# Performance work log

Hardware: AMD Instinct MI355X
Metric: run time of the kernel (lower is better)

Reference implementation:

```python
import jax, jax.numpy as jnp
import numpy as np

NEG_INF = -1e30

def setup_inputs() -> dict:
    key = jax.random.key(0)
    k1, k2, k3, k4, k5 = jax.random.split(key, 5)
    B, S, D, A = 16, 1024, 1024, 256
    hidden = jax.random.normal(k1, (B, S, D), dtype=jnp.float32)
    W1 = jax.random.normal(k2, (D, A), dtype=jnp.float32) / np.sqrt(D)
    b1 = jax.random.normal(k3, (A,), dtype=jnp.float32) * 0.01
    v = jax.random.normal(k4, (A,), dtype=jnp.float32) / np.sqrt(A)
    prompt_type_ids = jax.random.randint(k5, (B,), 0, 3, dtype=jnp.int32)
    return {"hidden": hidden, "W1": W1, "b1": b1, "v": v,
            "prompt_type_ids": prompt_type_ids}

def reference(hidden, W1, b1, v, prompt_type_ids):
    # hidden: [B,S,D]; per-token variable-length context attention pooling.
    B, S, D = hidden.shape
    # scores depend only on the context token l, not on the query position j
    attn_in = jnp.tanh(jnp.einsum('bsd,da->bsa', hidden, W1) + b1)  # [B,S,A]
    scores = jnp.einsum('bsa,a->bs', attn_in, v)                    # [B,S]

    idx = jnp.arange(S)
    j = idx[:, None]   # query position
    l = idx[None, :]   # context position
    prefix_m = l <= j          # h[:j+1]
    postfix_m = l >= j         # h[j:]
    cloze_m = l != j           # leave-one-out
    pt = prompt_type_ids[:, None, None]                              # [B,1,1]
    mask = jnp.where(pt == 0, prefix_m[None],
                     jnp.where(pt == 1, postfix_m[None], cloze_m[None]))  # [B,S,S] bool

    masked_scores = jnp.where(mask, scores[:, None, :], NEG_INF)    # [B,S(j),S(l)]
    p = jax.nn.softmax(masked_scores, axis=-1)                      # softmax over context
    cnt = jnp.sum(mask, axis=-1).astype(hidden.dtype)               # context length L per (b,j)
    # output = (1/L) * sum_l p_l * h_l  (the original's mean of p_l*h_l rows)
    pooled = jnp.einsum('bjl,bld->bjd', p, hidden) / cnt[..., None]
    return pooled
```

## Files before the change

### kernel.cpp

```cpp
#include <hip/hip_runtime.h>
#include <math.h>

#define SS 1024
#define DD 1024
#define AA 256
#define BB 16

typedef short short8 __attribute__((ext_vector_type(8)));
typedef short short4v __attribute__((ext_vector_type(4)));
typedef float f32x4 __attribute__((ext_vector_type(4)));

static __device__ __forceinline__ short f2bf(float f) {
    union { float f; unsigned u; } x; x.f = f;
    unsigned r = x.u + 0x7FFFu + ((x.u >> 16) & 1u);
    return (short)(r >> 16);
}

__global__ __launch_bounds__(256) void w1cvt_kernel(
    const float* __restrict__ W1, short* __restrict__ W1f)
{
    const int g  = blockIdx.x * 256 + threadIdx.x;
    const int l  = g & 63;
    const int nb = (g >> 6) & 15;
    const int kb = g >> 10;
    const int k0 = kb * 32 + ((l >> 4) << 3);
    const int n  = nb * 16 + (l & 15);
    short8 o;
    #pragma unroll
    for (int j = 0; j < 8; ++j) o[j] = f2bf(W1[(size_t)(k0 + j) * AA + n]);
    *reinterpret_cast<short8*>(&W1f[(size_t)g * 8]) = o;
}

__global__ __launch_bounds__(256) void scores_mfma_kernel(
    const float* __restrict__ hidden, const short* __restrict__ W1f,
    const float* __restrict__ b1, const float* __restrict__ v,
    float* __restrict__ scores)
{
    __shared__ short A_lds[32 * 32];
    __shared__ float red[4][32];

    const int tid = threadIdx.x;
    const int w   = tid >> 6;
    const int l   = tid & 63;
    const int row0 = blockIdx.x * 32;

    const int sr = tid >> 3;
    const int sc = (tid & 7) * 4;
    const float* hsrc = hidden + (size_t)(row0 + sr) * DD + sc;

    f32x4 acc[2][4];
    #pragma unroll
    for (int m = 0; m < 2; ++m)
        #pragma unroll
        for (int nb = 0; nb < 4; ++nb)
            #pragma unroll
            for (int r = 0; r < 4; ++r) acc[m][nb][r] = 0.f;

    const int a_off0 = (l & 15) * 32 + ((l >> 4) << 3);
    const short8* w1f8 = reinterpret_cast<const short8*>(W1f);

    for (int kb = 0; kb < 32; ++kb) {
        __syncthreads();
        const float4 hv = *reinterpret_cast<const float4*>(hsrc + kb * 32);
        short4v o;
        o[0] = f2bf(hv.x); o[1] = f2bf(hv.y); o[2] = f2bf(hv.z); o[3] = f2bf(hv.w);
        *reinterpret_cast<short4v*>(&A_lds[sr * 32 + sc]) = o;
        __syncthreads();

        const short8 a0 = *reinterpret_cast<const short8*>(&A_lds[a_off0]);
        const short8 a1 = *reinterpret_cast<const short8*>(&A_lds[a_off0 + 16 * 32]);
        const short8* bp = w1f8 + (size_t)(kb * 16 + w * 4) * 64 + l;
        #pragma unroll
        for (int nb = 0; nb < 4; ++nb) {
            const short8 bfr = bp[nb * 64];
            acc[0][nb] = __builtin_amdgcn_mfma_f32_16x16x32_bf16(a0, bfr, acc[0][nb], 0, 0, 0);
            acc[1][nb] = __builtin_amdgcn_mfma_f32_16x16x32_bf16(a1, bfr, acc[1][nb], 0, 0, 0);
        }
    }

    float b1l[4], vl[4];
    #pragma unroll
    for (int nb = 0; nb < 4; ++nb) {
        const int col = w * 64 + nb * 16 + (l & 15);
        b1l[nb] = b1[col];
        vl[nb]  = v[col];
    }
    #pragma unroll
    for (int m = 0; m < 2; ++m) {
        #pragma unroll
        for (int r = 0; r < 4; ++r) {
            float s = tanhf(acc[m][0][r] + b1l[0]) * vl[0]
                    + tanhf(acc[m][1][r] + b1l[1]) * vl[1]
                    + tanhf(acc[m][2][r] + b1l[2]) * vl[2]
                    + tanhf(acc[m][3][r] + b1l[3]) * vl[3];
            s += __shfl_xor(s, 1, 64);
            s += __shfl_xor(s, 2, 64);
            s += __shfl_xor(s, 4, 64);
            s += __shfl_xor(s, 8, 64);
            if ((l & 15) == 0) red[w][m * 16 + ((l >> 4) << 2) + r] = s;
        }
    }
    __syncthreads();
    if (tid < 32)
        scores[row0 + tid] = red[0][tid] + red[1][tid] + red[2][tid] + red[3][tid];
}

__global__ __launch_bounds__(1024) void prep_kernel(
    const float* __restrict__ scores, const int* __restrict__ pt,
    float* __restrict__ e_out, float* __restrict__ iv_out)
{
    __shared__ float red[1024];
    __shared__ float buf[1024];
    const int b   = blockIdx.x;
    const int tid = threadIdx.x;

    const float s = scores[b * SS + tid];
    red[tid] = s;
    __syncthreads();
    for (int off = 512; off > 0; off >>= 1) {
        if (tid < off) red[tid] = fmaxf(red[tid], red[tid + off]);
        __syncthreads();
    }
    const float m = red[0];
    __syncthreads();

    const float e = expf(s - m);
    e_out[b * SS + tid] = e;

    buf[tid] = e;
    __syncthreads();
    for (int off = 1; off < 1024; off <<= 1) {
        float val = buf[tid];
        if (tid >= off) val += buf[tid - off];
        __syncthreads();
        buf[tid] = val;
        __syncthreads();
    }
    const float P = buf[tid];
    const float Z = buf[1023];

    const int type = pt[b];
    float iv;
    if (type == 0)        iv = 1.f / (P * (float)(tid + 1));
    else if (type == 1)   iv = 1.f / ((Z - P + e) * (float)(SS - tid));
    else                  iv = 1.f / ((Z - e) * (float)(SS - 1));
    iv_out[b * SS + tid] = iv;
}

__global__ __launch_bounds__(1024) void pool_kernel(
    const float* __restrict__ hidden, const float* __restrict__ e_in,
    const float* __restrict__ iv_in, const int* __restrict__ pt,
    float* __restrict__ out)
{
    __shared__ float e_s[1024];
    __shared__ float iv_s[1024];
    __shared__ float seg[16][64];

    const int tid  = threadIdx.x;
    const int wave = tid >> 6;
    const int lane = tid & 63;
    const int b    = blockIdx.x >> 4;
    const int d    = (blockIdx.x & 15) * 64 + lane;

    e_s [tid] = e_in [b * SS + tid];
    iv_s[tid] = iv_in[b * SS + tid];
    __syncthreads();

    const float* hb = hidden + (size_t)b * SS * DD + d;
    float*       ob = out    + (size_t)b * SS * DD + d;
    const int l0 = wave * 64;

    float a0 = 0.f, a1 = 0.f, a2 = 0.f, a3 = 0.f;
    #pragma unroll
    for (int i = 0; i < 64; i += 4) {
        const int j = l0 + i;
        a0 += e_s[j + 0] * hb[(size_t)(j + 0) * DD];
        a1 += e_s[j + 1] * hb[(size_t)(j + 1) * DD];
        a2 += e_s[j + 2] * hb[(size_t)(j + 2) * DD];
        a3 += e_s[j + 3] * hb[(size_t)(j + 3) * DD];
    }
    seg[wave][lane] = (a0 + a1) + (a2 + a3);
    __syncthreads();

    const int type = pt[b];
    if (type == 0) {
        float run = 0.f;
        for (int w = 0; w < wave; ++w) run += seg[w][lane];
        #pragma unroll 4
        for (int i = 0; i < 64; ++i) {
            const int j = l0 + i;
            run += e_s[j] * hb[(size_t)j * DD];
            ob[(size_t)j * DD] = run * iv_s[j];
        }
    } else if (type == 1) {
        float run = 0.f;
        for (int w = wave + 1; w < 16; ++w) run += seg[w][lane];
        #pragma unroll 4
        for (int i = 63; i >= 0; --i) {
            const int j = l0 + i;
            run += e_s[j] * hb[(size_t)j * DD];
            ob[(size_t)j * DD] = run * iv_s[j];
        }
    } else {
        float T = 0.f;
        #pragma unroll
        for (int w = 0; w < 16; ++w) T += seg[w][lane];
        #pragma unroll 4
        for (int i = 0; i < 64; ++i) {
            const int j = l0 + i;
            ob[(size_t)j * DD] = (T - e_s[j] * hb[(size_t)j * DD]) * iv_s[j];
        }
    }
}

extern "C" void kernel_launch(void* const* d_in, const int* in_sizes, int n_in,
                              void* d_out, int out_size, void* d_ws, size_t ws_size,
                              hipStream_t stream) {
    const float* hidden = (const float*)d_in[0];
    const float* W1     = (const float*)d_in[1];
    const float* b1     = (const float*)d_in[2];
    const float* v      = (const float*)d_in[3];
    const int*   pt     = (const int*)  d_in[4];
    float* out = (float*)d_out;

    float* ws     = (float*)d_ws;
    float* scores = ws;
    float* e      = ws + BB * SS;
    float* iv     = ws + 2 * BB * SS;
    short* W1f    = (short*)(ws + 3 * BB * SS);

    w1cvt_kernel      <<<128, 256, 0, stream>>>(W1, W1f);
    scores_mfma_kernel<<<(BB * SS) / 32, 256, 0, stream>>>(hidden, W1f, b1, v, scores);
    prep_kernel       <<<BB, 1024, 0, stream>>>(scores, pt, e, iv);
    pool_kernel       <<<BB * (DD / 64), 1024, 0, stream>>>(hidden, e, iv, pt, out);
}
```

Measured before the change: 184.9 us.

## Fuse softmax prep into pool kernel and drop LDS staging in scores GEMM

The separate prep kernel goes away. Each pool block now recomputes the max, exp and prefix sums for its batch row with wave shuffles, which removes one launch and the e/iv round trip through global memory. The scores kernel loads A fragments straight from global and converts them in registers, so the LDS staging and the two barriers per k-step disappear. It uses 16-row tiles, which doubles the block count and also doubles W1 reads. Output stores are made nontemporal, and the bf16 conversion now uses the library intrinsic.

```diff
diff --git a/kernel.cpp b/kernel.cpp
--- a/kernel.cpp
+++ b/kernel.cpp
@@ -1,4 +1,5 @@
 #include <hip/hip_runtime.h>
+#include <hip/hip_bf16.h>
 #include <math.h>
 
 #define SS 1024
@@ -7,13 +8,12 @@
 #define BB 16
 
 typedef short short8 __attribute__((ext_vector_type(8)));
-typedef short short4v __attribute__((ext_vector_type(4)));
 typedef float f32x4 __attribute__((ext_vector_type(4)));
 
 static __device__ __forceinline__ short f2bf(float f) {
-    union { float f; unsigned u; } x; x.f = f;
-    unsigned r = x.u + 0x7FFFu + ((x.u >> 16) & 1u);
-    return (short)(r >> 16);
+    __hip_bfloat16 h = __float2bfloat16(f);
+    union { __hip_bfloat16 h; short s; } u; u.h = h;
+    return u.s;
 }
 
 __global__ __launch_bounds__(256) void w1cvt_kernel(
@@ -36,46 +36,33 @@
     const float* __restrict__ b1, const float* __restrict__ v,
     float* __restrict__ scores)
 {
-    __shared__ short A_lds[32 * 32];
-    __shared__ float red[4][32];
+    __shared__ float red[4][16];
 
     const int tid = threadIdx.x;
     const int w   = tid >> 6;
     const int l   = tid & 63;
-    const int row0 = blockIdx.x * 32;
-
-    const int sr = tid >> 3;
-    const int sc = (tid & 7) * 4;
-    const float* hsrc = hidden + (size_t)(row0 + sr) * DD + sc;
-
-    f32x4 acc[2][4];
-    #pragma unroll
-    for (int m = 0; m < 2; ++m)
+    const int row0 = blockIdx.x * 16;
+
+    const float*  ap = hidden + (size_t)(row0 + (l & 15)) * DD + ((l >> 4) << 3);
+    const short8* bp = reinterpret_cast<const short8*>(W1f) + (size_t)(w * 4) * 64 + l;
+
+    f32x4 acc[4];
+    #pragma unroll
+    for (int nb = 0; nb < 4; ++nb)
+        #pragma unroll
+        for (int r = 0; r < 4; ++r) acc[nb][r] = 0.f;
+
+    #pragma unroll 2
+    for (int kb = 0; kb < 32; ++kb) {
+        const float4 av0 = *reinterpret_cast<const float4*>(ap + kb * 32);
+        const float4 av1 = *reinterpret_cast<const float4*>(ap + kb * 32 + 4);
+        short8 a;
+        a[0] = f2bf(av0.x); a[1] = f2bf(av0.y); a[2] = f2bf(av0.z); a[3] = f2bf(av0.w);
+        a[4] = f2bf(av1.x); a[5] = f2bf(av1.y); a[6] = f2bf(av1.z); a[7] = f2bf(av1.w);
+        const short8* bkp = bp + (size_t)kb * 16 * 64;
         #pragma unroll
         for (int nb = 0; nb < 4; ++nb)
-            #pragma unroll
-            for (int r = 0; r < 4; ++r) acc[m][nb][r] = 0.f;
-
-    const int a_off0 = (l & 15) * 32 + ((l >> 4) << 3);
-    const short8* w1f8 = reinterpret_cast<const short8*>(W1f);
-
-    for (int kb = 0; kb < 32; ++kb) {
-        __syncthreads();
-        const float4 hv = *reinterpret_cast<const float4*>(hsrc + kb * 32);
-        short4v o;
-        o[0] = f2bf(hv.x); o[1] = f2bf(hv.y); o[2] = f2bf(hv.z); o[3] = f2bf(hv.w);
-        *reinterpret_cast<short4v*>(&A_lds[sr * 32 + sc]) = o;
-        __syncthreads();
-
-        const short8 a0 = *reinterpret_cast<const short8*>(&A_lds[a_off0]);
-        const short8 a1 = *reinterpret_cast<const short8*>(&A_lds[a_off0 + 16 * 32]);
-        const short8* bp = w1f8 + (size_t)(kb * 16 + w * 4) * 64 + l;
-        #pragma unroll
-        for (int nb = 0; nb < 4; ++nb) {
-            const short8 bfr = bp[nb * 64];
-            acc[0][nb] = __builtin_amdgcn_mfma_f32_16x16x32_bf16(a0, bfr, acc[0][nb], 0, 0, 0);
-            acc[1][nb] = __builtin_amdgcn_mfma_f32_16x16x32_bf16(a1, bfr, acc[1][nb], 0, 0, 0);
-        }
+            acc[nb] = __builtin_amdgcn_mfma_f32_16x16x32_bf16(a, bkp[nb * 64], acc[nb], 0, 0, 0);
     }
 
     float b1l[4], vl[4];
@@ -86,84 +73,73 @@
         vl[nb]  = v[col];
     }
     #pragma unroll
-    for (int m = 0; m < 2; ++m) {
-        #pragma unroll
-        for (int r = 0; r < 4; ++r) {
-            float s = tanhf(acc[m][0][r] + b1l[0]) * vl[0]
-                    + tanhf(acc[m][1][r] + b1l[1]) * vl[1]
-                    + tanhf(acc[m][2][r] + b1l[2]) * vl[2]
-                    + tanhf(acc[m][3][r] + b1l[3]) * vl[3];
-            s += __shfl_xor(s, 1, 64);
-            s += __shfl_xor(s, 2, 64);
-            s += __shfl_xor(s, 4, 64);
-            s += __shfl_xor(s, 8, 64);
-            if ((l & 15) == 0) red[w][m * 16 + ((l >> 4) << 2) + r] = s;
-        }
-    }
-    __syncthreads();
-    if (tid < 32)
+    for (int r = 0; r < 4; ++r) {
+        float s = tanhf(acc[0][r] + b1l[0]) * vl[0]
+                + tanhf(acc[1][r] + b1l[1]) * vl[1]
+                + tanhf(acc[2][r] + b1l[2]) * vl[2]
+                + tanhf(acc[3][r] + b1l[3]) * vl[3];
+        s += __shfl_xor(s, 1, 64);
+        s += __shfl_xor(s, 2, 64);
+        s += __shfl_xor(s, 4, 64);
+        s += __shfl_xor(s, 8, 64);
+        if ((l & 15) == 0) red[w][((l >> 4) << 2) + r] = s;
+    }
+    __syncthreads();
+    if (tid < 16)
         scores[row0 + tid] = red[0][tid] + red[1][tid] + red[2][tid] + red[3][tid];
 }
 
-__global__ __launch_bounds__(1024) void prep_kernel(
-    const float* __restrict__ scores, const int* __restrict__ pt,
-    float* __restrict__ e_out, float* __restrict__ iv_out)
+__global__ __launch_bounds__(1024) void pool_kernel(
+    const float* __restrict__ hidden, const float* __restrict__ scores,
+    const int* __restrict__ pt, float* __restrict__ out)
 {
-    __shared__ float red[1024];
-    __shared__ float buf[1024];
-    const int b   = blockIdx.x;
-    const int tid = threadIdx.x;
+    __shared__ float e_s[1024];
+    __shared__ float iv_s[1024];
+    __shared__ float seg[16][64];
+    __shared__ float wmax[16];
+    __shared__ float wsum[16];
+
+    const int tid  = threadIdx.x;
+    const int wave = tid >> 6;
+    const int lane = tid & 63;
+    const int b    = blockIdx.x >> 4;
+    const int d    = (blockIdx.x & 15) * 64 + lane;
 
     const float s = scores[b * SS + tid];
-    red[tid] = s;
-    __syncthreads();
-    for (int off = 512; off > 0; off >>= 1) {
-        if (tid < off) red[tid] = fmaxf(red[tid], red[tid + off]);
-        __syncthreads();
-    }
-    const float m = red[0];
-    __syncthreads();
+    float mx = s;
+    #pragma unroll
+    for (int off = 32; off > 0; off >>= 1) mx = fmaxf(mx, __shfl_xor(mx, off, 64));
+    if (lane == 0) wmax[wave] = mx;
+    __syncthreads();
+    float m = wmax[0];
+    #pragma unroll
+    for (int i = 1; i < 16; ++i) m = fmaxf(m, wmax[i]);
 
     const float e = expf(s - m);
-    e_out[b * SS + tid] = e;
-
-    buf[tid] = e;
-    __syncthreads();
-    for (int off = 1; off < 1024; off <<= 1) {
-        float val = buf[tid];
-        if (tid >= off) val += buf[tid - off];
-        __syncthreads();
-        buf[tid] = val;
-        __syncthreads();
-    }
-    const float P = buf[tid];
-    const float Z = buf[1023];
+    float ps = e;
+    #pragma unroll
+    for (int off = 1; off < 64; off <<= 1) {
+        const float t = __shfl_up(ps, off, 64);
+        if (lane >= off) ps += t;
+    }
+    if (lane == 63) wsum[wave] = ps;
+    __syncthreads();
+    float pre = 0.f, Z = 0.f;
+    #pragma unroll
+    for (int i = 0; i < 16; ++i) {
+        const float t = wsum[i];
+        if (i < wave) pre += t;
+        Z += t;
+    }
+    const float P = ps + pre;
 
     const int type = pt[b];
     float iv;
     if (type == 0)        iv = 1.f / (P * (float)(tid + 1));
     else if (type == 1)   iv = 1.f / ((Z - P + e) * (float)(SS - tid));
     else                  iv = 1.f / ((Z - e) * (float)(SS - 1));
-    iv_out[b * SS + tid] = iv;
-}
-
-__global__ __launch_bounds__(1024) void pool_kernel(
-    const float* __restrict__ hidden, const float* __restrict__ e_in,
-    const float* __restrict__ iv_in, const int* __restrict__ pt,
-    float* __restrict__ out)
-{
-    __shared__ float e_s[1024];
-    __shared__ float iv_s[1024];
-    __shared__ float seg[16][64];
-
-    const int tid  = threadIdx.x;
-    const int wave = tid >> 6;
-    const int lane = tid & 63;
-    const int b    = blockIdx.x >> 4;
-    const int d    = (blockIdx.x & 15) * 64 + lane;
-
-    e_s [tid] = e_in [b * SS + tid];
-    iv_s[tid] = iv_in[b * SS + tid];
+    e_s[tid]  = e;
+    iv_s[tid] = iv;
     __syncthreads();
 
     const float* hb = hidden + (size_t)b * SS * DD + d;
@@ -182,33 +158,33 @@
     seg[wave][lane] = (a0 + a1) + (a2 + a3);
     __syncthreads();
 
-    const int type = pt[b];
     if (type == 0) {
         float run = 0.f;
-        for (int w = 0; w < wave; ++w) run += seg[w][lane];
+        for (int w2 = 0; w2 < wave; ++w2) run += seg[w2][lane];
         #pragma unroll 4
         for (int i = 0; i < 64; ++i) {
             const int j = l0 + i;
             run += e_s[j] * hb[(size_t)j * DD];
-            ob[(size_t)j * DD] = run * iv_s[j];
+            __builtin_nontemporal_store(run * iv_s[j], &ob[(size_t)j * DD]);
         }
     } else if (type == 1) {
         float run = 0.f;
-        for (int w = wave + 1; w < 16; ++w) run += seg[w][lane];
+        for (int w2 = wave + 1; w2 < 16; ++w2) run += seg[w2][lane];
         #pragma unroll 4
         for (int i = 63; i >= 0; --i) {
             const int j = l0 + i;
             run += e_s[j] * hb[(size_t)j * DD];
-            ob[(size_t)j * DD] = run * iv_s[j];
+            __builtin_nontemporal_store(run * iv_s[j], &ob[(size_t)j * DD]);
         }
     } else {
         float T = 0.f;
         #pragma unroll
-        for (int w = 0; w < 16; ++w) T += seg[w][lane];
+        for (int w2 = 0; w2 < 16; ++w2) T += seg[w2][lane];
         #pragma unroll 4
         for (int i = 0; i < 64; ++i) {
             const int j = l0 + i;
-            ob[(size_t)j * DD] = (T - e_s[j] * hb[(size_t)j * DD]) * iv_s[j];
+            __builtin_nontemporal_store((T - e_s[j] * hb[(size_t)j * DD]) * iv_s[j],
+                                        &ob[(size_t)j * DD]);
         }
     }
 }
@@ -225,12 +201,9 @@
 
     float* ws     = (float*)d_ws;
     float* scores = ws;
-    float* e      = ws + BB * SS;
-    float* iv     = ws + 2 * BB * SS;
-    short* W1f    = (short*)(ws + 3 * BB * SS);
+    short* W1f    = (short*)(ws + BB * SS);
 
     w1cvt_kernel      <<<128, 256, 0, stream>>>(W1, W1f);
-    scores_mfma_kernel<<<(BB * SS) / 32, 256, 0, stream>>>(hidden, W1f, b1, v, scores);
-    prep_kernel       <<<BB, 1024, 0, stream>>>(scores, pt, e, iv);
-    pool_kernel       <<<BB * (DD / 64), 1024, 0, stream>>>(hidden, e, iv, pt, out);
-}
+    scores_mfma_kernel<<<(BB * SS) / 16, 256, 0, stream>>>(hidden, W1f, b1, v, scores);
+    pool_kernel       <<<BB * (DD / 64), 1024, 0, stream>>>(hidden, scores, pt, out);
+}
```

Result: faster. 179.7 us (-2.8%).
